# Optimization experiments

Measured on AMD Instinct MI355X. Metric: run time of the kernel, lower is better.

Reference implementation:

```python
import jax, jax.numpy as jnp
import numpy as np

NUM_ITERATIONS = 5
NUM_TERMS = 3  # (degree + 1) // 2 with degree = 5
INITIAL_SCALE = 1.1


def setup_inputs() -> dict:
    key = jax.random.key(0)
    k1, k2 = jax.random.split(key)
    X = jax.random.normal(k1, (64, 1024, 1024), dtype=jnp.float32)
    coefficients = jnp.array([3.4445, -4.7750, 2.0315], dtype=jnp.float32)
    return {"X": X, "coefficients": coefficients}


def reference(X, coefficients):
    # Normalize each matrix to Frobenius norm INITIAL_SCALE
    fro = jnp.sqrt(jnp.sum(X * X, axis=(-2, -1), keepdims=True))
    X = X / fro * INITIAL_SCALE
    for _ in range(NUM_ITERATIONS):
        # XTX = X^T X, shape [B, M, M]
        XTX = jnp.einsum('bji,bjk->bik', X, X)
        term = X
        acc = coefficients[0] * X
        for i in range(1, NUM_TERMS):
            term = jnp.einsum('bij,bjk->bik', term, XTX)  # X (X^T X)^i
            acc = acc + coefficients[i] * term
        X = acc
    return X
```

## Files before the change

kernel.cpp:

```cpp
#include <hip/hip_runtime.h>
#include <hip/hip_bf16.h>
#include <stdint.h>

typedef float f32x4 __attribute__((ext_vector_type(4)));
typedef short bf16x8 __attribute__((ext_vector_type(8)));

#define LDW 1024
#define BATCH_SH 20

__device__ __forceinline__ float b2f(__hip_bfloat16 h) { return __bfloat162float(h); }
__device__ __forceinline__ __hip_bfloat16 f2b(float f) { return __float2bfloat16(f); }

__device__ __forceinline__ void gload16(const void* g, void* l) {
  __builtin_amdgcn_global_load_lds((const __attribute__((address_space(1))) void*)g,
                                   (__attribute__((address_space(3))) void*)l,
                                   16, 0, 0);
}

__global__ void k_partial(const float* __restrict__ xin, float* __restrict__ partials) {
  const int b = blockIdx.y, ch = blockIdx.x, t = threadIdx.x;
  const size_t base = ((size_t)b << BATCH_SH) + (size_t)ch * 16384;
  float s = 0.f;
#pragma unroll
  for (int i = 0; i < 16; ++i) {
    f32x4 v = *reinterpret_cast<const f32x4*>(xin + base + (size_t)(i * 256 + t) * 4);
    s += v[0] * v[0] + v[1] * v[1] + v[2] * v[2] + v[3] * v[3];
  }
#pragma unroll
  for (int off = 32; off; off >>= 1) s += __shfl_down(s, off);
  __shared__ float red[4];
  if ((t & 63) == 0) red[t >> 6] = s;
  __syncthreads();
  if (t == 0) partials[b * 64 + ch] = red[0] + red[1] + red[2] + red[3];
}

__global__ void k_scale(const float* __restrict__ partials, float* __restrict__ scales) {
  const int b = blockIdx.x, t = threadIdx.x;
  float s = partials[b * 64 + t];
#pragma unroll
  for (int off = 32; off; off >>= 1) s += __shfl_down(s, off);
  if (t == 0) scales[b] = 1.1f / sqrtf(s);
}

__global__ void k_scalesplit(const float* __restrict__ xin, const float* __restrict__ scales,
                             __hip_bfloat16* __restrict__ Xh, __hip_bfloat16* __restrict__ Xl,
                             __hip_bfloat16* __restrict__ XTh, __hip_bfloat16* __restrict__ XTl) {
  __shared__ float tile[64][65];
  const int b = blockIdx.z, tm = blockIdx.y, tn = blockIdx.x;
  const size_t boff = (size_t)b << BATCH_SH;
  const float s = scales[b];
  const int t = threadIdx.x, lr0 = t >> 6, lc = t & 63;
#pragma unroll
  for (int p = 0; p < 16; ++p) {
    const int lr = p * 4 + lr0;
    const size_t idx = boff + (size_t)(tm * 64 + lr) * LDW + tn * 64 + lc;
    const float v = xin[idx] * s;
    __hip_bfloat16 h = f2b(v);
    Xh[idx] = h;
    Xl[idx] = f2b(v - b2f(h));
    tile[lr][lc] = v;
  }
  __syncthreads();
#pragma unroll
  for (int p = 0; p < 16; ++p) {
    const int lr = p * 4 + lr0;
    const float v = tile[lc][lr];
    const size_t idx = boff + (size_t)(tn * 64 + lr) * LDW + tm * 64 + lc;
    __hip_bfloat16 h = f2b(v);
    XTh[idx] = h;
    XTl[idx] = f2b(v - b2f(h));
  }
}


#define SEGPTRS(S)                                                                        \
  const int seg_ = (S) >> 4, k0_ = ((S) & 15) << 6;                                       \
  const __hip_bfloat16* pa_ = seg_ == 0 ? pa0 : seg_ == 1 ? pa1 : pa2;                    \
  const __hip_bfloat16* pb_ = seg_ == 0 ? pb0 : seg_ == 1 ? pb1 : pb2;

#define STAGE_GL(DB, S)                                                                   \
  {                                                                                       \
    SEGPTRS(S)                                                                            \
    char* lb_ = smem + (DB) * 65536;                                                      \
    _Pragma("unroll") for (int it_ = 0; it_ < 4; ++it_) {                                 \
      const int r_ = it_ * 64 + w * 8 + (l >> 3);                                         \
      const int kx_ = k0_ + (((l & 7) ^ (l >> 3)) << 3);                                  \
      gload16(pa_ + boff + (size_t)(rowA + r_) * LDW + kx_,                               \
              lb_ + (it_ * 64 + w * 8) * 128 + l * 16);                                   \
      gload16(pb_ + boff + (size_t)(rowB + r_) * LDW + kx_,                               \
              lb_ + 32768 + (it_ * 64 + w * 8) * 128 + l * 16);                           \
    }                                                                                     \
  }

#define MFMA_PHASE(KK, BASE)                                                              \
  {                                                                                       \
    bf16x8 av[8], bv[4];                                                                  \
    _Pragma("unroll") for (int mi_ = 0; mi_ < 8; ++mi_)                                   \
        av[mi_] = *reinterpret_cast<const bf16x8*>(smem + (BASE) + offA[KK][mi_]);        \
    _Pragma("unroll") for (int ni_ = 0; ni_ < 4; ++ni_)                                   \
        bv[ni_] = *reinterpret_cast<const bf16x8*>(smem + (BASE) + offB[KK][ni_]);        \
    __builtin_amdgcn_s_setprio(1);                                                        \
    _Pragma("unroll") for (int mi_ = 0; mi_ < 8; ++mi_)                                   \
        _Pragma("unroll") for (int ni_ = 0; ni_ < 4; ++ni_)                               \
            acc[mi_][ni_] = __builtin_amdgcn_mfma_f32_16x16x32_bf16(                      \
                av[mi_], bv[ni_], acc[mi_][ni_], 0, 0, 0);                                \
    __builtin_amdgcn_s_setprio(0);                                                        \
  }

template <int MODE>
__global__ __launch_bounds__(512, 2) void k_gemm(
    const __hip_bfloat16* __restrict__ pa0, const __hip_bfloat16* __restrict__ pa1,
    const __hip_bfloat16* __restrict__ pa2, const __hip_bfloat16* __restrict__ pb0,
    const __hip_bfloat16* __restrict__ pb1, const __hip_bfloat16* __restrict__ pb2,
    __hip_bfloat16* oh, __hip_bfloat16* ol,
    __hip_bfloat16* oth, __hip_bfloat16* otl,
    float* __restrict__ of,
    const __hip_bfloat16* __restrict__ eh, const __hip_bfloat16* __restrict__ el,
    const float* __restrict__ coef) {
  __shared__ __align__(16) char smem[131072];
  const int t = threadIdx.x;
  const int w = t >> 6, l = t & 63;
  const int wr = w >> 2, wc = w & 3;

  const int nwg = gridDim.x, q = nwg >> 3, r8 = nwg & 7;
  const int xcd = blockIdx.x & 7, o = blockIdx.x >> 3;
  const int wgid = (xcd < r8 ? xcd * (q + 1) : r8 * (q + 1) + (xcd - r8) * q) + o;

  int bat, tm, tn;
  if constexpr (MODE == 3) {
    bat = wgid >> 4;
    const int tile = wgid & 15;
    tm = tile >> 2; tn = tile & 3;
  } else {
    bat = (int)((unsigned)wgid / 10u);
    const int tile = wgid - bat * 10;
    tm = (tile < 4) ? 0 : (tile < 7) ? 1 : (tile < 9) ? 2 : 3;
    tn = (tile < 4) ? tile : (tile < 7) ? (tile - 3) : (tile < 9) ? (tile - 5) : 3;
  }
  const size_t boff = (size_t)bat << BATCH_SH;
  const int rowA = tm * 256, rowB = tn * 256;

  f32x4 acc[8][4];
#pragma unroll
  for (int i = 0; i < 8; ++i)
#pragma unroll
    for (int j = 0; j < 4; ++j) acc[i][j] = (f32x4){0.f, 0.f, 0.f, 0.f};

  int offA[2][8], offB[2][4];
#pragma unroll
  for (int kk = 0; kk < 2; ++kk) {
    const int g = kk * 4 + (l >> 4);
#pragma unroll
    for (int mi = 0; mi < 8; ++mi) {
      const int rA = wr * 128 + mi * 16 + (l & 15);
      offA[kk][mi] = rA * 128 + ((g ^ (rA & 7)) << 4);
    }
#pragma unroll
    for (int ni = 0; ni < 4; ++ni) {
      const int rB = wc * 64 + ni * 16 + (l & 15);
      offB[kk][ni] = 32768 + rB * 128 + ((g ^ (rB & 7)) << 4);
    }
  }

  STAGE_GL(0, 0);
  asm volatile("s_waitcnt vmcnt(0)" ::: "memory");
  __builtin_amdgcn_sched_barrier(0);
  __builtin_amdgcn_s_barrier();
  __builtin_amdgcn_sched_barrier(0);

  for (int s = 0; s < 48; ++s) {
    const int base = (s & 1) * 65536;
    if (s + 1 < 48) STAGE_GL((s & 1) ^ 1, s + 1);
    __builtin_amdgcn_sched_barrier(0);
    MFMA_PHASE(0, base);
    MFMA_PHASE(1, base);
    asm volatile("s_waitcnt vmcnt(0) lgkmcnt(0)" ::: "memory");
    __builtin_amdgcn_sched_barrier(0);
    __builtin_amdgcn_s_barrier();
    __builtin_amdgcn_sched_barrier(0);
  }

  float c0 = 0.f, c1 = 0.f, c2 = 0.f;
  if constexpr (MODE == 2) { c0 = coef[0]; c1 = coef[1]; c2 = coef[2]; }
  const int r0 = tm * 256 + wr * 128 + ((l >> 4) << 2);
  const int cb = tn * 256 + wc * 64 + (l & 15);
#pragma unroll
  for (int mi = 0; mi < 8; ++mi) {
#pragma unroll
    for (int ni = 0; ni < 4; ++ni) {
      const int ccol = cb + ni * 16;
#pragma unroll
      for (int j = 0; j < 4; ++j) {
        const int rrow = r0 + mi * 16 + j;
        const size_t idx = boff + (size_t)rrow * LDW + ccol;
        const size_t tix = boff + (size_t)ccol * LDW + rrow;
        float v = acc[mi][ni][j];
        if constexpr (MODE == 2)
          v = c2 * v + c1 * (b2f(eh[idx]) + b2f(el[idx])) + (rrow == ccol ? c0 : 0.f);
        __hip_bfloat16 h = f2b(v);
        __hip_bfloat16 lo = f2b(v - b2f(h));
        if constexpr (MODE == 3) {
          if (oh) {
            oh[idx] = h; ol[idx] = lo;
            oth[tix] = h; otl[tix] = lo;
          }
          if (of) of[idx] = v;
        } else {
          oh[idx] = h; ol[idx] = lo;
          if (tm != tn) { oth[tix] = h; otl[tix] = lo; }
        }
      }
    }
  }
}

extern "C" void kernel_launch(void* const* d_in, const int* in_sizes, int n_in,
                              void* d_out, int out_size, void* d_ws, size_t ws_size,
                              hipStream_t stream) {
  (void)in_sizes; (void)n_in; (void)out_size;
  const float* xin = (const float*)d_in[0];
  const float* coef = (const float*)d_in[1];
  float* xout = (float*)d_out;

  int CH = 64;
  while (CH > 1 && ((size_t)CH * 16u * 1024u * 1024u + 65536u) > ws_size) CH >>= 1;

  const size_t nE = (size_t)CH << BATCH_SH;
  __hip_bfloat16* P0h = (__hip_bfloat16*)d_ws;
  __hip_bfloat16* P0l = P0h + nE;
  __hip_bfloat16* P1h = P0l + nE;
  __hip_bfloat16* P1l = P1h + nE;
  __hip_bfloat16* P2h = P1l + nE;
  __hip_bfloat16* P2l = P2h + nE;
  __hip_bfloat16* XTh = P2l + nE;
  __hip_bfloat16* XTl = XTh + nE;
  float* partials = (float*)(XTl + nE);
  float* scales = partials + (size_t)CH * 64;

  for (int c = 0; c < 64; c += CH) {
    const float* xi = xin + ((size_t)c << BATCH_SH);
    float* X = xout + ((size_t)c << BATCH_SH);
    k_partial<<<dim3(64, CH), 256, 0, stream>>>(xi, partials);
    k_scale<<<dim3(CH), 64, 0, stream>>>(partials, scales);
    k_scalesplit<<<dim3(16, 16, CH), 256, 0, stream>>>(xi, scales, P0h, P0l, XTh, XTl);

    __hip_bfloat16 *Xh = P0h, *Xl = P0l, *Ah = P1h, *Al = P1l, *Bh = P2h, *Bl = P2l;
    for (int it = 0; it < 5; ++it) {
      k_gemm<1><<<dim3(CH * 10), 512, 0, stream>>>(XTh, XTh, XTl, XTh, XTl, XTh,
                                                   Ah, Al, Ah, Al, nullptr,
                                                   nullptr, nullptr, nullptr);
      k_gemm<2><<<dim3(CH * 10), 512, 0, stream>>>(Ah, Ah, Al, Ah, Al, Ah,
                                                   Bh, Bl, Bh, Bl, nullptr,
                                                   Ah, Al, coef);
      k_gemm<3><<<dim3(CH * 16), 512, 0, stream>>>(Xh, Xh, Xl, Bh, Bl, Bh,
                                                   (it < 4) ? Ah : nullptr,
                                                   (it < 4) ? Al : nullptr,
                                                   XTh, XTl,
                                                   (it == 4) ? X : nullptr,
                                                   nullptr, nullptr, nullptr);
      __hip_bfloat16 *th = Xh, *tl = Xl;
      Xh = Ah; Xl = Al;
      Ah = Bh; Al = Bl;
      Bh = th; Bl = tl;
    }
  }
}
```

Before: 7.895 ms.

## Stage transposed X output through LDS for coalesced stores; fold scale kernel

```diff
diff --git a/kernel.cpp b/kernel.cpp
--- a/kernel.cpp
+++ b/kernel.cpp
@@ -34,22 +34,18 @@
   if (t == 0) partials[b * 64 + ch] = red[0] + red[1] + red[2] + red[3];
 }
 
-__global__ void k_scale(const float* __restrict__ partials, float* __restrict__ scales) {
-  const int b = blockIdx.x, t = threadIdx.x;
-  float s = partials[b * 64 + t];
-#pragma unroll
-  for (int off = 32; off; off >>= 1) s += __shfl_down(s, off);
-  if (t == 0) scales[b] = 1.1f / sqrtf(s);
-}
-
-__global__ void k_scalesplit(const float* __restrict__ xin, const float* __restrict__ scales,
+__global__ void k_scalesplit(const float* __restrict__ xin, const float* __restrict__ partials,
                              __hip_bfloat16* __restrict__ Xh, __hip_bfloat16* __restrict__ Xl,
                              __hip_bfloat16* __restrict__ XTh, __hip_bfloat16* __restrict__ XTl) {
   __shared__ float tile[64][65];
   const int b = blockIdx.z, tm = blockIdx.y, tn = blockIdx.x;
   const size_t boff = (size_t)b << BATCH_SH;
-  const float s = scales[b];
   const int t = threadIdx.x, lr0 = t >> 6, lc = t & 63;
+  float q = partials[b * 64 + (t & 63)];
+#pragma unroll
+  for (int off = 32; off; off >>= 1) q += __shfl_down(q, off);
+  q = __shfl(q, 0);
+  const float s = 1.1f / sqrtf(q);
 #pragma unroll
   for (int p = 0; p < 16; ++p) {
     const int lr = p * 4 + lr0;
@@ -193,21 +189,69 @@
       for (int j = 0; j < 4; ++j) {
         const int rrow = r0 + mi * 16 + j;
         const size_t idx = boff + (size_t)rrow * LDW + ccol;
-        const size_t tix = boff + (size_t)ccol * LDW + rrow;
         float v = acc[mi][ni][j];
         if constexpr (MODE == 2)
           v = c2 * v + c1 * (b2f(eh[idx]) + b2f(el[idx])) + (rrow == ccol ? c0 : 0.f);
         __hip_bfloat16 h = f2b(v);
         __hip_bfloat16 lo = f2b(v - b2f(h));
         if constexpr (MODE == 3) {
-          if (oh) {
-            oh[idx] = h; ol[idx] = lo;
-            oth[tix] = h; otl[tix] = lo;
-          }
+          if (oh) { oh[idx] = h; ol[idx] = lo; }
           if (of) of[idx] = v;
         } else {
           oh[idx] = h; ol[idx] = lo;
-          if (tm != tn) { oth[tix] = h; otl[tix] = lo; }
+          if (tm != tn) {
+            const size_t tix = boff + (size_t)ccol * LDW + rrow;
+            oth[tix] = h; otl[tix] = lo;
+          }
+        }
+      }
+    }
+  }
+
+  if constexpr (MODE == 3) {
+    if (oth) {
+      unsigned* tlds = reinterpret_cast<unsigned*>(smem);
+      unsigned short* pth = reinterpret_cast<unsigned short*>(oth);
+      unsigned short* ptl = reinterpret_cast<unsigned short*>(otl);
+#pragma unroll
+      for (int h2 = 0; h2 < 2; ++h2) {
+        __builtin_amdgcn_s_barrier();
+        if ((wc >> 1) == h2) {
+#pragma unroll
+          for (int mi = 0; mi < 8; ++mi) {
+#pragma unroll
+            for (int ni = 0; ni < 4; ++ni) {
+              const int cl = (wc & 1) * 64 + ni * 16 + (l & 15);
+#pragma unroll
+              for (int j = 0; j < 4; ++j) {
+                const int rr = wr * 128 + ((l >> 4) << 2) + mi * 16 + j;
+                const float v = acc[mi][ni][j];
+                const __hip_bfloat16 hh = f2b(v);
+                const __hip_bfloat16 lo = f2b(v - b2f(hh));
+                const unsigned pk = (unsigned)(*(const unsigned short*)&hh) |
+                                    ((unsigned)(*(const unsigned short*)&lo) << 16);
+                tlds[rr * 128 + (cl ^ ((rr >> 1) & 31))] = pk;
+              }
+            }
+          }
+        }
+        __builtin_amdgcn_s_barrier();
+#pragma unroll
+        for (int i = 0; i < 16; ++i) {
+          const int trow = w * 16 + i;
+          const size_t obase =
+              boff + (size_t)(tn * 256 + h2 * 128 + trow) * LDW + tm * 256;
+#pragma unroll
+          for (int c = 0; c < 2; ++c) {
+            const int e0 = (c * 64 + l) * 2;
+            const int m = (e0 >> 1) & 31;
+            const unsigned p0 = tlds[e0 * 128 + (trow ^ m)];
+            const unsigned p1 = tlds[(e0 + 1) * 128 + (trow ^ m)];
+            *reinterpret_cast<unsigned*>(pth + obase + e0) =
+                (p0 & 0xffffu) | (p1 << 16);
+            *reinterpret_cast<unsigned*>(ptl + obase + e0) =
+                (p0 >> 16) | (p1 & 0xffff0000u);
+          }
         }
       }
     }
@@ -235,14 +279,12 @@
   __hip_bfloat16* XTh = P2l + nE;
   __hip_bfloat16* XTl = XTh + nE;
   float* partials = (float*)(XTl + nE);
-  float* scales = partials + (size_t)CH * 64;
 
   for (int c = 0; c < 64; c += CH) {
     const float* xi = xin + ((size_t)c << BATCH_SH);
     float* X = xout + ((size_t)c << BATCH_SH);
     k_partial<<<dim3(64, CH), 256, 0, stream>>>(xi, partials);
-    k_scale<<<dim3(CH), 64, 0, stream>>>(partials, scales);
-    k_scalesplit<<<dim3(16, 16, CH), 256, 0, stream>>>(xi, scales, P0h, P0l, XTh, XTl);
+    k_scalesplit<<<dim3(16, 16, CH), 256, 0, stream>>>(xi, partials, P0h, P0l, XTh, XTl);
 
     __hip_bfloat16 *Xh = P0h, *Xl = P0l, *Ah = P1h, *Al = P1l, *Bh = P2h, *Bl = P2l;
     for (int it = 0; it < 5; ++it) {
@@ -255,7 +297,8 @@
       k_gemm<3><<<dim3(CH * 16), 512, 0, stream>>>(Xh, Xh, Xl, Bh, Bl, Bh,
                                                    (it < 4) ? Ah : nullptr,
                                                    (it < 4) ? Al : nullptr,
-                                                   XTh, XTl,
+                                                   (it < 4) ? XTh : nullptr,
+                                                   (it < 4) ? XTl : nullptr,
                                                    (it == 4) ? X : nullptr,
                                                    nullptr, nullptr, nullptr);
       __hip_bfloat16 *th = Xh, *tl = Xl;
```

New measurement: 7.440 ms. 5.8% less time.
